# Kernel tuning notes

Measured on AMD Instinct MI355X. Metric: run time of the kernel, lower is better.

## Reference

```python
import jax, jax.numpy as jnp
import numpy as np

B, S, K, D = 128, 64, 10, 256
THR = -1.5


def setup_inputs() -> dict:
    key = jax.random.key(0)
    ks = jax.random.split(key, 9)
    si = 1.0 / np.sqrt(D)  # torch GRU init: U(-1/sqrt(hidden), 1/sqrt(hidden))
    u = lambda k, shape, s: jax.random.uniform(k, shape, jnp.float32, -s, s)
    return {
        "item_embs": jax.random.normal(ks[0], (B, S, K, D), jnp.float32),
        "user_embs": jax.random.normal(ks[1], (B, S, D), jnp.float32),
        "W_ih": u(ks[2], (3 * D, 2 * D), si),
        "W_hh": u(ks[3], (3 * D, D), si),
        "b_ih": u(ks[4], (3 * D,), si),
        "b_hh": u(ks[5], (3 * D,), si),
        "w_out": u(ks[6], (D,), si),
        "b_out": u(ks[7], (), si),
        "length": jax.random.randint(ks[8], (B,), 0, S),
    }


def reference(item_embs, user_embs, W_ih, W_hh, b_ih, b_hh, w_out, b_out, length):
    N = B * S
    # x['items'] = cat([item_embs.flatten(0,1), zeros_like(...)], -1)  -> [N, K, 2D]
    items_flat = item_embs.reshape(N, K, D)
    items = jnp.concatenate([items_flat, jnp.zeros_like(items_flat)], axis=-1)
    # user hidden state: gather user_embs at (length-1, clamped), repeat over S
    idx = jnp.clip(length - 1, 0, None)  # [B]
    u0 = user_embs[jnp.arange(B), idx]   # [B, D]
    h0 = jnp.repeat(u0, S, axis=0)       # [N, D]

    def gru_cell(x, h):
        gi = x @ W_ih.T + b_ih  # [N, 3D]
        gh = h @ W_hh.T + b_hh
        i_r, i_z, i_n = jnp.split(gi, 3, axis=-1)
        h_r, h_z, h_n = jnp.split(gh, 3, axis=-1)
        r = jax.nn.sigmoid(i_r + h_r)
        z = jax.nn.sigmoid(i_z + h_z)
        n = jnp.tanh(i_n + r * h_n)
        return (1.0 - z) * n + z * h

    def step(carry, x_t):
        h, mask = carry  # mask [N,1]: readout threshold gate for the click-half of input
        x = jnp.concatenate([x_t[:, :D], x_t[:, D:] * mask], axis=-1)
        h = gru_cell(x, h)
        y = h @ w_out + b_out  # [N]
        next_mask = (jax.lax.stop_gradient(y) > THR).astype(x_t.dtype)[:, None]
        return (h, next_mask), y

    xs = jnp.swapaxes(items, 0, 1)  # [K, N, 2D]
    init = (h0, jnp.ones((N, 1), item_embs.dtype))
    _, ys = jax.lax.scan(step, init, xs)  # ys [K, N]
    y = jnp.swapaxes(ys, 0, 1)  # [N, K]
    # self.w = 1, self.b = 0 -> identity calibration
    return y.reshape(B, S, K)
```

## Files before the change

### kernel.cpp

```cpp
#include <hip/hip_runtime.h>

#define BB 128
#define SS 64
#define KK 10
#define DD 256
#define NN (BB*SS)
#define ROWS 32
#define NBLK (NN/ROWS)
#define NT 512

typedef __attribute__((ext_vector_type(8))) short short8;
typedef __attribute__((ext_vector_type(4))) float f32x4;

#define FRAG_ELEMS (48*8*64*8)

__device__ __forceinline__ unsigned short f2bf(float f){
  union { float f; unsigned u; } v; v.f = f;
  unsigned r = (v.u + 0x7FFFu + ((v.u >> 16) & 1u)) >> 16;
  return (unsigned short)r;
}

__global__ void prep_weights(const float* __restrict__ Wih,
                             const float* __restrict__ Whh,
                             unsigned short* __restrict__ fw){
  int id = blockIdx.x * 256 + threadIdx.x;
  int arr = (id >= FRAG_ELEMS);
  int r = arr ? (id - FRAG_ELEMS) : id;
  int j  = r & 7;
  int l  = (r >> 3) & 63;
  int tk = (r >> 9) & 7;
  int tn = r >> 12;
  int c  = tn * 16 + (l & 15);
  int d  = tk * 32 + ((l >> 4) << 3) + j;
  float v = arr ? Whh[c * 256 + d] : Wih[c * 512 + d];
  fw[id] = f2bf(v);
}

__global__ __launch_bounds__(NT, 2) void gru_main(
    const float* __restrict__ item, const float* __restrict__ user,
    const float* __restrict__ b_ih, const float* __restrict__ b_hh,
    const float* __restrict__ w_out, const float* __restrict__ b_out,
    const int* __restrict__ length, const unsigned short* __restrict__ ws,
    float* __restrict__ out)
{
  __shared__ unsigned short xfrag[2*8*64*8];
  __shared__ unsigned short hfrag[2*8*64*8];
  __shared__ float yp[8][2][4][4];

  const int tid  = threadIdx.x;
  const int lane = tid & 63;
  const int w    = tid >> 6;
  const int col  = lane & 15;
  const int q    = lane >> 4;
  const int nb   = blockIdx.x * ROWS;
  const int b    = nb / SS;

  const short8* fw1 = (const short8*)ws;
  const short8* fwh = fw1 + (FRAG_ELEMS/8);

  float br_[2], bz_[2], bin_[2], bhn_[2], wo_[2];
  #pragma unroll
  for (int gi = 0; gi < 2; ++gi){
    int d = (w*2 + gi)*16 + col;
    br_[gi]  = b_ih[d]       + b_hh[d];
    bz_[gi]  = b_ih[256 + d] + b_hh[256 + d];
    bin_[gi] = b_ih[512 + d];
    bhn_[gi] = b_hh[512 + d];
    wo_[gi]  = w_out[d];
  }

  int idx = length[b] - 1; if (idx < 0) idx = 0;
  float h[2][2][4];
  #pragma unroll
  for (int gi = 0; gi < 2; ++gi){
    float u0 = user[((size_t)b*SS + idx)*DD + (w*2 + gi)*16 + col];
    #pragma unroll
    for (int mt = 0; mt < 2; ++mt)
      #pragma unroll
      for (int reg = 0; reg < 4; ++reg)
        h[mt][gi][reg] = u0;
  }

  #pragma unroll
  for (int mt = 0; mt < 2; ++mt)
    #pragma unroll
    for (int gi = 0; gi < 2; ++gi){
      int d   = (w*2 + gi)*16 + col;
      int tkk = d >> 5;
      int slb = ((d >> 3) & 3) * 16;
      #pragma unroll
      for (int reg = 0; reg < 4; ++reg){
        int m = q*4 + reg;
        hfrag[((mt*8 + tkk)*64 + slb + m)*8 + (d & 7)] = f2bf(h[mt][gi][reg]);
      }
    }

  const int xrow = tid >> 4;
  const int xd0  = (tid & 15) * 16;
  {
    const float4* p = (const float4*)(item + ((size_t)(nb + xrow)*KK + 0)*DD + xd0);
    float4 xv0 = p[0], xv1 = p[1], xv2 = p[2], xv3 = p[3];
    unsigned short tmp[16];
    tmp[0]=f2bf(xv0.x); tmp[1]=f2bf(xv0.y); tmp[2]=f2bf(xv0.z); tmp[3]=f2bf(xv0.w);
    tmp[4]=f2bf(xv1.x); tmp[5]=f2bf(xv1.y); tmp[6]=f2bf(xv1.z); tmp[7]=f2bf(xv1.w);
    tmp[8]=f2bf(xv2.x); tmp[9]=f2bf(xv2.y); tmp[10]=f2bf(xv2.z); tmp[11]=f2bf(xv2.w);
    tmp[12]=f2bf(xv3.x); tmp[13]=f2bf(xv3.y); tmp[14]=f2bf(xv3.z); tmp[15]=f2bf(xv3.w);
    int m = xrow & 15, mt = xrow >> 4, o0 = (tid & 15)*2;
    #pragma unroll
    for (int oo = 0; oo < 2; ++oo){
      int o = o0 + oo, tkk = o >> 2, sl = (o & 3)*16 + m;
      *(short8*)&xfrag[((mt*8 + tkk)*64 + sl)*8] = *(short8*)&tmp[oo*8];
    }
  }
  __syncthreads();

  const float bout = b_out[0];

  for (int k = 0; k < KK; ++k){
    f32x4 acc[2][2][4];
    #pragma unroll
    for (int mt = 0; mt < 2; ++mt)
      #pragma unroll
      for (int gi = 0; gi < 2; ++gi)
        #pragma unroll
        for (int kd = 0; kd < 4; ++kd){
          f32x4 z4 = {0.f, 0.f, 0.f, 0.f};
          acc[mt][gi][kd] = z4;
        }

    #pragma unroll 2
    for (int tk = 0; tk < 8; ++tk){
      short8 ax[2], ah[2];
      #pragma unroll
      for (int mt = 0; mt < 2; ++mt){
        ax[mt] = *(const short8*)&xfrag[((mt*8 + tk)*64 + lane)*8];
        ah[mt] = *(const short8*)&hfrag[((mt*8 + tk)*64 + lane)*8];
      }
      #pragma unroll
      for (int gi = 0; gi < 2; ++gi){
        int g = w*2 + gi;
        short8 w1r = fw1[((g     )*8 + tk)*64 + lane];
        short8 w1z = fw1[((16 + g)*8 + tk)*64 + lane];
        short8 w1n = fw1[((32 + g)*8 + tk)*64 + lane];
        short8 whr = fwh[((g     )*8 + tk)*64 + lane];
        short8 whz = fwh[((16 + g)*8 + tk)*64 + lane];
        short8 whn = fwh[((32 + g)*8 + tk)*64 + lane];
        #pragma unroll
        for (int mt = 0; mt < 2; ++mt){
          acc[mt][gi][0] = __builtin_amdgcn_mfma_f32_16x16x32_bf16(ax[mt], w1r, acc[mt][gi][0], 0, 0, 0);
          acc[mt][gi][0] = __builtin_amdgcn_mfma_f32_16x16x32_bf16(ah[mt], whr, acc[mt][gi][0], 0, 0, 0);
          acc[mt][gi][1] = __builtin_amdgcn_mfma_f32_16x16x32_bf16(ax[mt], w1z, acc[mt][gi][1], 0, 0, 0);
          acc[mt][gi][1] = __builtin_amdgcn_mfma_f32_16x16x32_bf16(ah[mt], whz, acc[mt][gi][1], 0, 0, 0);
          acc[mt][gi][2] = __builtin_amdgcn_mfma_f32_16x16x32_bf16(ax[mt], w1n, acc[mt][gi][2], 0, 0, 0);
          acc[mt][gi][3] = __builtin_amdgcn_mfma_f32_16x16x32_bf16(ah[mt], whn, acc[mt][gi][3], 0, 0, 0);
        }
      }
    }

    float4 xn0, xn1, xn2, xn3;
    if (k < KK-1){
      const float4* p = (const float4*)(item + ((size_t)(nb + xrow)*KK + (k+1))*DD + xd0);
      xn0 = p[0]; xn1 = p[1]; xn2 = p[2]; xn3 = p[3];
    }

    float ypl[2][4];
    #pragma unroll
    for (int mt = 0; mt < 2; ++mt)
      #pragma unroll
      for (int reg = 0; reg < 4; ++reg) ypl[mt][reg] = 0.f;

    #pragma unroll
    for (int mt = 0; mt < 2; ++mt)
      #pragma unroll
      for (int gi = 0; gi < 2; ++gi)
        #pragma unroll
        for (int reg = 0; reg < 4; ++reg){
          float rp = acc[mt][gi][0][reg] + br_[gi];
          float zp = acc[mt][gi][1][reg] + bz_[gi];
          float r  = 1.f / (1.f + __expf(-rp));
          float z  = 1.f / (1.f + __expf(-zp));
          float np = acc[mt][gi][2][reg] + bin_[gi] + r*(acc[mt][gi][3][reg] + bhn_[gi]);
          np = fminf(fmaxf(np, -30.f), 30.f);
          float e  = __expf(2.f*np);
          float n  = (e - 1.f) / (e + 1.f);
          float hv = (1.f - z)*n + z*h[mt][gi][reg];
          h[mt][gi][reg] = hv;
          ypl[mt][reg] += hv * wo_[gi];
        }

    #pragma unroll
    for (int mt = 0; mt < 2; ++mt)
      #pragma unroll
      for (int reg = 0; reg < 4; ++reg){
        float p = ypl[mt][reg];
        p += __shfl_xor(p, 1);
        p += __shfl_xor(p, 2);
        p += __shfl_xor(p, 4);
        p += __shfl_xor(p, 8);
        if (col == 0) yp[w][mt][q][reg] = p;
      }

    __syncthreads();

    #pragma unroll
    for (int mt = 0; mt < 2; ++mt)
      #pragma unroll
      for (int gi = 0; gi < 2; ++gi){
        int d   = (w*2 + gi)*16 + col;
        int tkk = d >> 5;
        int slb = ((d >> 3) & 3) * 16;
        #pragma unroll
        for (int reg = 0; reg < 4; ++reg){
          int m = q*4 + reg;
          hfrag[((mt*8 + tkk)*64 + slb + m)*8 + (d & 7)] = f2bf(h[mt][gi][reg]);
        }
      }

    if (k < KK-1){
      unsigned short tmp[16];
      tmp[0]=f2bf(xn0.x); tmp[1]=f2bf(xn0.y); tmp[2]=f2bf(xn0.z); tmp[3]=f2bf(xn0.w);
      tmp[4]=f2bf(xn1.x); tmp[5]=f2bf(xn1.y); tmp[6]=f2bf(xn1.z); tmp[7]=f2bf(xn1.w);
      tmp[8]=f2bf(xn2.x); tmp[9]=f2bf(xn2.y); tmp[10]=f2bf(xn2.z); tmp[11]=f2bf(xn2.w);
      tmp[12]=f2bf(xn3.x); tmp[13]=f2bf(xn3.y); tmp[14]=f2bf(xn3.z); tmp[15]=f2bf(xn3.w);
      int m = xrow & 15, mt = xrow >> 4, o0 = (tid & 15)*2;
      #pragma unroll
      for (int oo = 0; oo < 2; ++oo){
        int o = o0 + oo, tkk = o >> 2, sl = (o & 3)*16 + m;
        *(short8*)&xfrag[((mt*8 + tkk)*64 + sl)*8] = *(short8*)&tmp[oo*8];
      }
    }

    if (tid < 32){
      float s = bout;
      #pragma unroll
      for (int ww = 0; ww < 8; ++ww)
        s += yp[ww][tid >> 4][(tid >> 2) & 3][tid & 3];
      out[(size_t)(nb + tid)*KK + k] = s;
    }

    __syncthreads();
  }
}

extern "C" void kernel_launch(void* const* d_in, const int* in_sizes, int n_in,
                              void* d_out, int out_size, void* d_ws, size_t ws_size,
                              hipStream_t stream) {
  const float* item   = (const float*)d_in[0];
  const float* user   = (const float*)d_in[1];
  const float* W_ih   = (const float*)d_in[2];
  const float* W_hh   = (const float*)d_in[3];
  const float* b_ih   = (const float*)d_in[4];
  const float* b_hh   = (const float*)d_in[5];
  const float* w_out  = (const float*)d_in[6];
  const float* b_out  = (const float*)d_in[7];
  const int*   length = (const int*)d_in[8];
  unsigned short* ws  = (unsigned short*)d_ws;
  float* out = (float*)d_out;

  hipLaunchKernelGGL(prep_weights, dim3((2*FRAG_ELEMS)/256), dim3(256), 0, stream,
                     W_ih, W_hh, ws);
  hipLaunchKernelGGL(gru_main, dim3(NBLK), dim3(NT), 0, stream,
                     item, user, b_ih, b_hh, w_out, b_out, length, ws, out);
}
```

Measured before the change: 249.2 us.

## Double-buffer x/h fragments, use 16 waves, and defer output reduction one step

Doubles the block to 1024 threads so each wave handles one 16-column gate slice instead of two, halving per-wave accumulators and weight loads. The x and h LDS fragments are double-buffered, which removes one of the two barriers per recurrence step. The output reduction is deferred one step using a triple-buffered partial-sum array. Per-wave MFMA work drops, but more waves now contend for the same LDS and weight-fetch bandwidth, and the launch-bounds occupancy target rises.

```diff
diff --git a/kernel.cpp b/kernel.cpp
--- a/kernel.cpp
+++ b/kernel.cpp
@@ -7,7 +7,7 @@
 #define NN (BB*SS)
 #define ROWS 32
 #define NBLK (NN/ROWS)
-#define NT 512
+#define NT 1024
 
 typedef __attribute__((ext_vector_type(8))) short short8;
 typedef __attribute__((ext_vector_type(4))) float f32x4;
@@ -36,16 +36,16 @@
   fw[id] = f2bf(v);
 }
 
-__global__ __launch_bounds__(NT, 2) void gru_main(
+__global__ __launch_bounds__(NT, 4) void gru_main(
     const float* __restrict__ item, const float* __restrict__ user,
     const float* __restrict__ b_ih, const float* __restrict__ b_hh,
     const float* __restrict__ w_out, const float* __restrict__ b_out,
     const int* __restrict__ length, const unsigned short* __restrict__ ws,
     float* __restrict__ out)
 {
-  __shared__ unsigned short xfrag[2*8*64*8];
-  __shared__ unsigned short hfrag[2*8*64*8];
-  __shared__ float yp[8][2][4][4];
+  __shared__ unsigned short xfrag[2][2*8*64*8];
+  __shared__ unsigned short hfrag[2][2*8*64*8];
+  __shared__ float yp[3][16][2][4][4];
 
   const int tid  = threadIdx.x;
   const int lane = tid & 63;
@@ -58,135 +58,113 @@
   const short8* fw1 = (const short8*)ws;
   const short8* fwh = fw1 + (FRAG_ELEMS/8);
 
-  float br_[2], bz_[2], bin_[2], bhn_[2], wo_[2];
-  #pragma unroll
-  for (int gi = 0; gi < 2; ++gi){
-    int d = (w*2 + gi)*16 + col;
-    br_[gi]  = b_ih[d]       + b_hh[d];
-    bz_[gi]  = b_ih[256 + d] + b_hh[256 + d];
-    bin_[gi] = b_ih[512 + d];
-    bhn_[gi] = b_hh[512 + d];
-    wo_[gi]  = w_out[d];
-  }
+  const int d    = w*16 + col;
+  const float br_  = b_ih[d]       + b_hh[d];
+  const float bz_  = b_ih[256 + d] + b_hh[256 + d];
+  const float bin_ = b_ih[512 + d];
+  const float bhn_ = b_hh[512 + d];
+  const float wo_  = w_out[d];
 
   int idx = length[b] - 1; if (idx < 0) idx = 0;
-  float h[2][2][4];
-  #pragma unroll
-  for (int gi = 0; gi < 2; ++gi){
-    float u0 = user[((size_t)b*SS + idx)*DD + (w*2 + gi)*16 + col];
-    #pragma unroll
-    for (int mt = 0; mt < 2; ++mt)
-      #pragma unroll
-      for (int reg = 0; reg < 4; ++reg)
-        h[mt][gi][reg] = u0;
-  }
-
+  const float u0 = user[((size_t)b*SS + idx)*DD + d];
+  float h[2][4];
   #pragma unroll
   for (int mt = 0; mt < 2; ++mt)
     #pragma unroll
-    for (int gi = 0; gi < 2; ++gi){
-      int d   = (w*2 + gi)*16 + col;
-      int tkk = d >> 5;
-      int slb = ((d >> 3) & 3) * 16;
-      #pragma unroll
-      for (int reg = 0; reg < 4; ++reg){
-        int m = q*4 + reg;
-        hfrag[((mt*8 + tkk)*64 + slb + m)*8 + (d & 7)] = f2bf(h[mt][gi][reg]);
+    for (int reg = 0; reg < 4; ++reg)
+      h[mt][reg] = u0;
+
+  const int tkk = d >> 5;
+  const int slb = ((d >> 3) & 3) * 16;
+  const int dj  = d & 7;
+  {
+    unsigned short hb = f2bf(u0);
+    #pragma unroll
+    for (int mt = 0; mt < 2; ++mt)
+      #pragma unroll
+      for (int reg = 0; reg < 4; ++reg)
+        hfrag[0][((mt*8 + tkk)*64 + slb + q*4 + reg)*8 + dj] = hb;
+  }
+
+  const int xrow = tid >> 5;
+  const int xo   = tid & 31;
+  const int xmt  = xrow >> 4;
+  const int xtk  = xo >> 2;
+  const int xsl  = (xo & 3)*16 + (xrow & 15);
+  {
+    const float4* p = (const float4*)(item + ((size_t)(nb + xrow)*KK + 0)*DD + xo*8);
+    float4 a0 = p[0], a1 = p[1];
+    unsigned short t[8];
+    t[0]=f2bf(a0.x); t[1]=f2bf(a0.y); t[2]=f2bf(a0.z); t[3]=f2bf(a0.w);
+    t[4]=f2bf(a1.x); t[5]=f2bf(a1.y); t[6]=f2bf(a1.z); t[7]=f2bf(a1.w);
+    *(short8*)&xfrag[0][((xmt*8 + xtk)*64 + xsl)*8] = *(short8*)t;
+  }
+  __syncthreads();
+
+  const float bout = b_out[0];
+
+  for (int k = 0; k < KK; ++k){
+    const int cb  = k & 1;
+    const int nbf = cb ^ 1;
+
+    f32x4 acc[2][4];
+    #pragma unroll
+    for (int mt = 0; mt < 2; ++mt)
+      #pragma unroll
+      for (int kd = 0; kd < 4; ++kd){
+        f32x4 z4 = {0.f, 0.f, 0.f, 0.f};
+        acc[mt][kd] = z4;
       }
-    }
-
-  const int xrow = tid >> 4;
-  const int xd0  = (tid & 15) * 16;
-  {
-    const float4* p = (const float4*)(item + ((size_t)(nb + xrow)*KK + 0)*DD + xd0);
-    float4 xv0 = p[0], xv1 = p[1], xv2 = p[2], xv3 = p[3];
-    unsigned short tmp[16];
-    tmp[0]=f2bf(xv0.x); tmp[1]=f2bf(xv0.y); tmp[2]=f2bf(xv0.z); tmp[3]=f2bf(xv0.w);
-    tmp[4]=f2bf(xv1.x); tmp[5]=f2bf(xv1.y); tmp[6]=f2bf(xv1.z); tmp[7]=f2bf(xv1.w);
-    tmp[8]=f2bf(xv2.x); tmp[9]=f2bf(xv2.y); tmp[10]=f2bf(xv2.z); tmp[11]=f2bf(xv2.w);
-    tmp[12]=f2bf(xv3.x); tmp[13]=f2bf(xv3.y); tmp[14]=f2bf(xv3.z); tmp[15]=f2bf(xv3.w);
-    int m = xrow & 15, mt = xrow >> 4, o0 = (tid & 15)*2;
-    #pragma unroll
-    for (int oo = 0; oo < 2; ++oo){
-      int o = o0 + oo, tkk = o >> 2, sl = (o & 3)*16 + m;
-      *(short8*)&xfrag[((mt*8 + tkk)*64 + sl)*8] = *(short8*)&tmp[oo*8];
-    }
-  }
-  __syncthreads();
-
-  const float bout = b_out[0];
-
-  for (int k = 0; k < KK; ++k){
-    f32x4 acc[2][2][4];
-    #pragma unroll
-    for (int mt = 0; mt < 2; ++mt)
-      #pragma unroll
-      for (int gi = 0; gi < 2; ++gi)
-        #pragma unroll
-        for (int kd = 0; kd < 4; ++kd){
-          f32x4 z4 = {0.f, 0.f, 0.f, 0.f};
-          acc[mt][gi][kd] = z4;
-        }
 
     #pragma unroll 2
     for (int tk = 0; tk < 8; ++tk){
-      short8 ax[2], ah[2];
-      #pragma unroll
-      for (int mt = 0; mt < 2; ++mt){
-        ax[mt] = *(const short8*)&xfrag[((mt*8 + tk)*64 + lane)*8];
-        ah[mt] = *(const short8*)&hfrag[((mt*8 + tk)*64 + lane)*8];
+      short8 ax0 = *(const short8*)&xfrag[cb][((0*8 + tk)*64 + lane)*8];
+      short8 ax1 = *(const short8*)&xfrag[cb][((1*8 + tk)*64 + lane)*8];
+      short8 ah0 = *(const short8*)&hfrag[cb][((0*8 + tk)*64 + lane)*8];
+      short8 ah1 = *(const short8*)&hfrag[cb][((1*8 + tk)*64 + lane)*8];
+      short8 w1r = fw1[((w     )*8 + tk)*64 + lane];
+      short8 w1z = fw1[((16 + w)*8 + tk)*64 + lane];
+      short8 w1n = fw1[((32 + w)*8 + tk)*64 + lane];
+      short8 whr = fwh[((w     )*8 + tk)*64 + lane];
+      short8 whz = fwh[((16 + w)*8 + tk)*64 + lane];
+      short8 whn = fwh[((32 + w)*8 + tk)*64 + lane];
+      acc[0][0] = __builtin_amdgcn_mfma_f32_16x16x32_bf16(ax0, w1r, acc[0][0], 0, 0, 0);
+      acc[0][0] = __builtin_amdgcn_mfma_f32_16x16x32_bf16(ah0, whr, acc[0][0], 0, 0, 0);
+      acc[0][1] = __builtin_amdgcn_mfma_f32_16x16x32_bf16(ax0, w1z, acc[0][1], 0, 0, 0);
+      acc[0][1] = __builtin_amdgcn_mfma_f32_16x16x32_bf16(ah0, whz, acc[0][1], 0, 0, 0);
+      acc[0][2] = __builtin_amdgcn_mfma_f32_16x16x32_bf16(ax0, w1n, acc[0][2], 0, 0, 0);
+      acc[0][3] = __builtin_amdgcn_mfma_f32_16x16x32_bf16(ah0, whn, acc[0][3], 0, 0, 0);
+      acc[1][0] = __builtin_amdgcn_mfma_f32_16x16x32_bf16(ax1, w1r, acc[1][0], 0, 0, 0);
+      acc[1][0] = __builtin_amdgcn_mfma_f32_16x16x32_bf16(ah1, whr, acc[1][0], 0, 0, 0);
+      acc[1][1] = __builtin_amdgcn_mfma_f32_16x16x32_bf16(ax1, w1z, acc[1][1], 0, 0, 0);
+      acc[1][1] = __builtin_amdgcn_mfma_f32_16x16x32_bf16(ah1, whz, acc[1][1], 0, 0, 0);
+      acc[1][2] = __builtin_amdgcn_mfma_f32_16x16x32_bf16(ax1, w1n, acc[1][2], 0, 0, 0);
+      acc[1][3] = __builtin_amdgcn_mfma_f32_16x16x32_bf16(ah1, whn, acc[1][3], 0, 0, 0);
+    }
+
+    float4 xn0, xn1;
+    if (k < KK-1){
+      const float4* p = (const float4*)(item + ((size_t)(nb + xrow)*KK + (k+1))*DD + xo*8);
+      xn0 = p[0]; xn1 = p[1];
+    }
+
+    float ypl[2][4];
+    #pragma unroll
+    for (int mt = 0; mt < 2; ++mt)
+      #pragma unroll
+      for (int reg = 0; reg < 4; ++reg){
+        float rp = acc[mt][0][reg] + br_;
+        float zp = acc[mt][1][reg] + bz_;
+        float r  = 1.f / (1.f + __expf(-rp));
+        float z  = 1.f / (1.f + __expf(-zp));
+        float np = acc[mt][2][reg] + bin_ + r*(acc[mt][3][reg] + bhn_);
+        np = fminf(fmaxf(np, -30.f), 30.f);
+        float e  = __expf(2.f*np);
+        float n  = (e - 1.f) / (e + 1.f);
+        float hv = (1.f - z)*n + z*h[mt][reg];
+        h[mt][reg] = hv;
+        ypl[mt][reg] = hv * wo_;
       }
-      #pragma unroll
-      for (int gi = 0; gi < 2; ++gi){
-        int g = w*2 + gi;
-        short8 w1r = fw1[((g     )*8 + tk)*64 + lane];
-        short8 w1z = fw1[((16 + g)*8 + tk)*64 + lane];
-        short8 w1n = fw1[((32 + g)*8 + tk)*64 + lane];
-        short8 whr = fwh[((g     )*8 + tk)*64 + lane];
-        short8 whz = fwh[((16 + g)*8 + tk)*64 + lane];
-        short8 whn = fwh[((32 + g)*8 + tk)*64 + lane];
-        #pragma unroll
-        for (int mt = 0; mt < 2; ++mt){
-          acc[mt][gi][0] = __builtin_amdgcn_mfma_f32_16x16x32_bf16(ax[mt], w1r, acc[mt][gi][0], 0, 0, 0);
-          acc[mt][gi][0] = __builtin_amdgcn_mfma_f32_16x16x32_bf16(ah[mt], whr, acc[mt][gi][0], 0, 0, 0);
-          acc[mt][gi][1] = __builtin_amdgcn_mfma_f32_16x16x32_bf16(ax[mt], w1z, acc[mt][gi][1], 0, 0, 0);
-          acc[mt][gi][1] = __builtin_amdgcn_mfma_f32_16x16x32_bf16(ah[mt], whz, acc[mt][gi][1], 0, 0, 0);
-          acc[mt][gi][2] = __builtin_amdgcn_mfma_f32_16x16x32_bf16(ax[mt], w1n, acc[mt][gi][2], 0, 0, 0);
-          acc[mt][gi][3] = __builtin_amdgcn_mfma_f32_16x16x32_bf16(ah[mt], whn, acc[mt][gi][3], 0, 0, 0);
-        }
-      }
-    }
-
-    float4 xn0, xn1, xn2, xn3;
-    if (k < KK-1){
-      const float4* p = (const float4*)(item + ((size_t)(nb + xrow)*KK + (k+1))*DD + xd0);
-      xn0 = p[0]; xn1 = p[1]; xn2 = p[2]; xn3 = p[3];
-    }
-
-    float ypl[2][4];
-    #pragma unroll
-    for (int mt = 0; mt < 2; ++mt)
-      #pragma unroll
-      for (int reg = 0; reg < 4; ++reg) ypl[mt][reg] = 0.f;
-
-    #pragma unroll
-    for (int mt = 0; mt < 2; ++mt)
-      #pragma unroll
-      for (int gi = 0; gi < 2; ++gi)
-        #pragma unroll
-        for (int reg = 0; reg < 4; ++reg){
-          float rp = acc[mt][gi][0][reg] + br_[gi];
-          float zp = acc[mt][gi][1][reg] + bz_[gi];
-          float r  = 1.f / (1.f + __expf(-rp));
-          float z  = 1.f / (1.f + __expf(-zp));
-          float np = acc[mt][gi][2][reg] + bin_[gi] + r*(acc[mt][gi][3][reg] + bhn_[gi]);
-          np = fminf(fmaxf(np, -30.f), 30.f);
-          float e  = __expf(2.f*np);
-          float n  = (e - 1.f) / (e + 1.f);
-          float hv = (1.f - z)*n + z*h[mt][gi][reg];
-          h[mt][gi][reg] = hv;
-          ypl[mt][reg] += hv * wo_[gi];
-        }
 
     #pragma unroll
     for (int mt = 0; mt < 2; ++mt)
@@ -197,48 +175,39 @@
         p += __shfl_xor(p, 2);
         p += __shfl_xor(p, 4);
         p += __shfl_xor(p, 8);
-        if (col == 0) yp[w][mt][q][reg] = p;
+        if (col == 0) yp[k % 3][w][mt][q][reg] = p;
       }
 
+    #pragma unroll
+    for (int mt = 0; mt < 2; ++mt)
+      #pragma unroll
+      for (int reg = 0; reg < 4; ++reg)
+        hfrag[nbf][((mt*8 + tkk)*64 + slb + q*4 + reg)*8 + dj] = f2bf(h[mt][reg]);
+
+    if (k < KK-1){
+      unsigned short t[8];
+      t[0]=f2bf(xn0.x); t[1]=f2bf(xn0.y); t[2]=f2bf(xn0.z); t[3]=f2bf(xn0.w);
+      t[4]=f2bf(xn1.x); t[5]=f2bf(xn1.y); t[6]=f2bf(xn1.z); t[7]=f2bf(xn1.w);
+      *(short8*)&xfrag[nbf][((xmt*8 + xtk)*64 + xsl)*8] = *(short8*)t;
+    }
+
+    if (k > 0 && tid < 32){
+      float s = bout;
+      #pragma unroll
+      for (int ww = 0; ww < 16; ++ww)
+        s += yp[(k-1) % 3][ww][tid >> 4][(tid >> 2) & 3][tid & 3];
+      out[(size_t)(nb + tid)*KK + (k-1)] = s;
+    }
+
     __syncthreads();
-
-    #pragma unroll
-    for (int mt = 0; mt < 2; ++mt)
-      #pragma unroll
-      for (int gi = 0; gi < 2; ++gi){
-        int d   = (w*2 + gi)*16 + col;
-        int tkk = d >> 5;
-        int slb = ((d >> 3) & 3) * 16;
-        #pragma unroll
-        for (int reg = 0; reg < 4; ++reg){
-          int m = q*4 + reg;
-          hfrag[((mt*8 + tkk)*64 + slb + m)*8 + (d & 7)] = f2bf(h[mt][gi][reg]);
-        }
-      }
-
-    if (k < KK-1){
-      unsigned short tmp[16];
-      tmp[0]=f2bf(xn0.x); tmp[1]=f2bf(xn0.y); tmp[2]=f2bf(xn0.z); tmp[3]=f2bf(xn0.w);
-      tmp[4]=f2bf(xn1.x); tmp[5]=f2bf(xn1.y); tmp[6]=f2bf(xn1.z); tmp[7]=f2bf(xn1.w);
-      tmp[8]=f2bf(xn2.x); tmp[9]=f2bf(xn2.y); tmp[10]=f2bf(xn2.z); tmp[11]=f2bf(xn2.w);
-      tmp[12]=f2bf(xn3.x); tmp[13]=f2bf(xn3.y); tmp[14]=f2bf(xn3.z); tmp[15]=f2bf(xn3.w);
-      int m = xrow & 15, mt = xrow >> 4, o0 = (tid & 15)*2;
-      #pragma unroll
-      for (int oo = 0; oo < 2; ++oo){
-        int o = o0 + oo, tkk = o >> 2, sl = (o & 3)*16 + m;
-        *(short8*)&xfrag[((mt*8 + tkk)*64 + sl)*8] = *(short8*)&tmp[oo*8];
-      }
-    }
-
-    if (tid < 32){
-      float s = bout;
-      #pragma unroll
-      for (int ww = 0; ww < 8; ++ww)
-        s += yp[ww][tid >> 4][(tid >> 2) & 3][tid & 3];
-      out[(size_t)(nb + tid)*KK + k] = s;
-    }
-
-    __syncthreads();
+  }
+
+  if (tid < 32){
+    float s = bout;
+    #pragma unroll
+    for (int ww = 0; ww < 16; ++ww)
+      s += yp[(KK-1) % 3][ww][tid >> 4][(tid >> 2) & 3][tid & 3];
+    out[(size_t)(nb + tid)*KK + (KK-1)] = s;
   }
 }
 
```

New measurement: 230.1 us. 7.7% less time.
